# Optimization experiments

Measured on AMD Instinct MI355X. Metric: run time of the kernel, lower is better.

The kernel has to match this reference:

```python
import jax, jax.numpy as jnp
import numpy as np

BETA = 0.25


def setup_inputs() -> dict:
    key = jax.random.key(0)
    k1, k2 = jax.random.split(key)
    x = jax.random.normal(k1, (32, 64, 64, 64), dtype=jnp.float32)   # [B, C, H, W]
    emb = jax.random.normal(k2, (1024, 64), dtype=jnp.float32)       # [K, C] codebook
    return {"x": x, "emb": emb}


def reference(x, emb):
    b, c, h, w = x.shape
    # (b h w) c
    z = jnp.transpose(x, (0, 2, 3, 1)).reshape(-1, c)
    # squared euclidean distances (argmin identical to torch.cdist argmin)
    # ||z||^2 - 2 z e^T + ||e||^2, never taking sqrt since only argmin is used
    d = (jnp.sum(z * z, axis=1, keepdims=True)
         - 2.0 * jnp.einsum('nc,kc->nk', z, emb)
         + jnp.sum(emb * emb, axis=1)[None, :])        # [N, K]
    idx = jnp.argmin(d, axis=1)                        # [N] int
    e = emb[idx]                                       # gather [N, C]
    e = jnp.transpose(e.reshape(b, h, w, c), (0, 3, 1, 2))  # [B, C, H, W]
    codebook_loss = jnp.mean((jax.lax.stop_gradient(x) - e) ** 2)
    commitment_loss = BETA * jnp.mean((x - jax.lax.stop_gradient(e)) ** 2)
    loss = codebook_loss + commitment_loss
    o = x + jax.lax.stop_gradient(e - x)               # straight-through
    indices = idx.reshape(b, h, w)
    return (o, loss, indices)
```

## Files before the change

kernel.cpp:

```cpp
#include <hip/hip_runtime.h>

#define BATCH   32
#define CCH     64
#define HW      4096
#define NPIX    (BATCH * HW)
#define KCODES  1024
#define NELEM   (NPIX * CCH)
#define MB      256
#define CK      128
#define MARGIN_Q 3u

typedef _Float16 f16;
typedef __attribute__((ext_vector_type(8))) _Float16 f16x8;
typedef __attribute__((ext_vector_type(4))) float    f32x4;

static __device__ __forceinline__ f32x4 mfma16(f16x8 a, f16x8 b, f32x4 c) {
    return __builtin_amdgcn_mfma_f32_16x16x32_f16(a, b, c, 0, 0, 0);
}

static __device__ __forceinline__ void dma16(void* lds, const void* g) {
    __builtin_amdgcn_global_load_lds(
        (const __attribute__((address_space(1))) unsigned int*)g,
        (__attribute__((address_space(3))) unsigned int*)lds, 16, 0, 0);
}

static __device__ __forceinline__ unsigned med3u(unsigned a, unsigned b, unsigned c) {
    unsigned d;
    asm("v_med3_u32 %0, %1, %2, %3" : "=v"(d) : "v"(a), "v"(b), "v"(c));
    return d;
}

#define WS_EEB_F   64
#define WS_CBH_B   8192
#define WS_CBL_B   139264
#define WS_WL_U    67584

__global__ __launch_bounds__(256) void vq_prep(
    const float* __restrict__ emb, float* __restrict__ wsf,
    unsigned* __restrict__ wsu, f16* __restrict__ cbH, f16* __restrict__ cbL,
    float* __restrict__ eeb_g)
{
    const int t   = threadIdx.x;
    const int gid = blockIdx.x * 256 + t;
    const int row = gid >> 3, gi = gid & 7;
    if (gid == 0) { wsf[0] = 0.f; wsu[1] = 0u; }
    const float* src = emb + (size_t)row * CCH + gi * 8;
    float4 v0 = *(const float4*)(src);
    float4 v1 = *(const float4*)(src + 4);
    float vv[8] = {v0.x, v0.y, v0.z, v0.w, v1.x, v1.y, v1.z, v1.w};
    f16x8 h, l;
    float s = 0.f;
#pragma unroll
    for (int j = 0; j < 8; ++j) {
        f16 hh = (f16)vv[j];
        h[j] = hh;
        l[j] = (f16)(vv[j] - (float)hh);
        s = fmaf(vv[j], vv[j], s);
    }
    const int off = row * 64 + 8 * (gi ^ (row & 7));
    *(f16x8*)(cbH + off) = h;
    *(f16x8*)(cbL + off) = l;
    s += __shfl_xor(s, 1, 64);
    s += __shfl_xor(s, 2, 64);
    s += __shfl_xor(s, 4, 64);
    if (gi == 0) eeb_g[row] = fmaf(s, 2048.0f, 1048576.0f);
}

__global__ __launch_bounds__(512, 4) void vq_main(
    const float* __restrict__ x,
    const float* __restrict__ emb,
    const f16* __restrict__ cbH, const f16* __restrict__ cbL,
    const float* __restrict__ eeb_g,
    float* __restrict__ o, float* __restrict__ idx_out,
    float* __restrict__ acc, unsigned* __restrict__ wl_count,
    unsigned* __restrict__ wl, unsigned cap)
{
    __shared__ __align__(16) char smem[65536];
    __shared__ float eebl[2][CK];
    __shared__ unsigned bu1[MB], bu2[MB];
    __shared__ float wred[8];

    const int t    = threadIdx.x;
    const int lane = t & 63;
    const int w    = t >> 6;
    const int col  = lane & 15;
    const int quad = lane >> 4;
    const int c7   = col & 7;
    const int sw0  = 8 * (quad ^ c7);
    const int sw1  = sw0 ^ 32;
    const int n0   = blockIdx.x * MB;
    const int b    = n0 >> 12;
    const int p0   = n0 & 4095;
    const float* xb = x + (size_t)b * (CCH * HW) + p0;

    auto stage = [&](int chunk, int bufi) {
        const int k0 = chunk * CK;
        char* lb = smem + bufi * 32768;
        const char* gH = (const char*)cbH + (size_t)k0 * 128 + w * 2048 + lane * 16;
        const char* gL = (const char*)cbL + (size_t)k0 * 128 + w * 2048 + lane * 16;
        char* lH = lb + w * 2048;
        char* lL = lb + 16384 + w * 2048;
        dma16(lH,        gH);
        dma16(lH + 1024, gH + 1024);
        dma16(lL,        gL);
        dma16(lL + 1024, gL + 1024);
        if (t < CK) eebl[bufi][t] = eeb_g[k0 + t];
    };

    stage(0, 0);

    f16x8 aH[2][2], aL[2][2];
#pragma unroll
    for (int rt = 0; rt < 2; ++rt) {
        const int pp = w * 32 + rt * 16 + col;
#pragma unroll
        for (int kc = 0; kc < 2; ++kc) {
            f16x8 h, l;
#pragma unroll
            for (int j = 0; j < 8; ++j) {
                const int c = kc * 32 + quad * 8 + j;
                float zs = -2.0f * xb[(size_t)c * HW + pp];
                f16 hh = (f16)zs;
                h[j] = hh;
                l[j] = (f16)(zs - (float)hh);
            }
            aH[rt][kc] = h;
            aL[rt][kc] = l;
        }
    }

    unsigned best[8], best2[8];
#pragma unroll
    for (int s = 0; s < 8; ++s) { best[s] = 0xFFFFFFFFu; best2[s] = 0xFFFFFFFFu; }

    const f32x4 zero4 = {0.f, 0.f, 0.f, 0.f};

    for (int chunk = 0; chunk < KCODES / CK; ++chunk) {
        const int cur = chunk & 1;
        __syncthreads();
        if (chunk + 1 < KCODES / CK) stage(chunk + 1, cur ^ 1);

        const f16* bufH = (const f16*)(smem + cur * 32768);
        const f16* bufL = bufH + 8192;
        const int k0 = chunk * CK;

#pragma unroll
        for (int tile = 0; tile < CK / 16; ++tile) {
            const f16* bh = bufH + (tile * 16 + col) * 64;
            const f16* bl = bufL + (tile * 16 + col) * 64;
            f16x8 bH0 = *(const f16x8*)(bh + sw0);
            f16x8 bH1 = *(const f16x8*)(bh + sw1);
            f16x8 bL0 = *(const f16x8*)(bl + sw0);
            f16x8 bL1 = *(const f16x8*)(bl + sw1);
            const float eebc = eebl[cur][tile * 16 + col];
            const unsigned kb = (unsigned)(k0 + tile * 16 + col);
#pragma unroll
            for (int rt = 0; rt < 2; ++rt) {
                f32x4 u = mfma16(aH[rt][0], bH0, zero4);
                f32x4 v = mfma16(aH[rt][1], bH1, zero4);
                u = mfma16(aL[rt][0], bH0, u);
                v = mfma16(aL[rt][1], bH1, v);
                u = mfma16(aH[rt][0], bL0, u);
                v = mfma16(aH[rt][1], bL1, v);
#pragma unroll
                for (int r = 0; r < 4; ++r) {
                    float uf = fmaf(u[r] + v[r], 2048.0f, eebc);
                    unsigned pk = (((unsigned)uf) << 10) | kb;
                    const int s = rt * 4 + r;
                    const unsigned b0 = best[s];
                    best2[s] = med3u(b0, best2[s], pk);
                    best[s]  = min(b0, pk);
                }
            }
        }
    }

#pragma unroll
    for (int d = 1; d < 16; d <<= 1) {
#pragma unroll
        for (int s = 0; s < 8; ++s) {
            unsigned ob  = __shfl_xor(best[s],  d, 64);
            unsigned ob2 = __shfl_xor(best2[s], d, 64);
            best2[s] = min(min(best2[s], ob2), max(best[s], ob));
            best[s]  = min(best[s], ob);
        }
    }
    if (col == 0) {
#pragma unroll
        for (int rt = 0; rt < 2; ++rt)
#pragma unroll
            for (int r = 0; r < 4; ++r) {
                const int pl = w * 32 + rt * 16 + quad * 4 + r;
                bu1[pl] = best[rt * 4 + r];
                bu2[pl] = best2[rt * 4 + r];
            }
    }
    __syncthreads();

    const int pix  = t & 255;
    const int half = t >> 8;
    const unsigned bu = bu1[pix];
    const unsigned bidx = bu & 1023u;
    if (half == 0) {
        idx_out[n0 + pix] = (float)bidx;
        const unsigned qg = (bu2[pix] >> 10) - (bu >> 10);
        if (qg < MARGIN_Q) {
            unsigned pos = atomicAdd(wl_count, 1u);
            if (pos < cap) wl[pos] = (unsigned)(n0 + pix);
        }
    }
    float ss = 0.f;
    {
        const float4* er4 = (const float4*)(emb + (size_t)bidx * CCH) + half * 8;
        const float* xbt = xb + pix;
        float* ob = o + (size_t)b * (CCH * HW) + p0 + pix;
#pragma unroll
        for (int i = 0; i < 8; ++i) {
            float4 ev = er4[i];
            float evv[4] = {ev.x, ev.y, ev.z, ev.w};
#pragma unroll
            for (int q = 0; q < 4; ++q) {
                const int c = half * 32 + i * 4 + q;
                float xv = xbt[(size_t)c * HW];
                float e  = evv[q];
                ob[(size_t)c * HW] = xv + (e - xv);
                float d = xv - e;
                ss = fmaf(d, d, ss);
            }
        }
    }
    for (int off = 32; off; off >>= 1) ss += __shfl_down(ss, off, 64);
    if (lane == 0) wred[w] = ss;
    __syncthreads();
    if (t == 0) {
        float s2 = 0.f;
#pragma unroll
        for (int q = 0; q < 8; ++q) s2 += wred[q];
        atomicAdd(acc, s2);
    }
}

__global__ __launch_bounds__(256) void vq_refine(
    const float* __restrict__ x, const float* __restrict__ emb,
    float* __restrict__ o, float* __restrict__ idx_out,
    float* __restrict__ acc, const unsigned* __restrict__ wl_count,
    const unsigned* __restrict__ wl, unsigned cap)
{
    __shared__ float zsh[CCH];
    __shared__ double rbd[4];
    __shared__ int rbi[4];
    __shared__ int s_pk;
    unsigned cnt = *wl_count; if (cnt > cap) cnt = cap;
    const int t = threadIdx.x;

    for (unsigned i = blockIdx.x; i < cnt; i += gridDim.x) {
        const int n = (int)wl[i];
        const int b = n >> 12, p = n & 4095;
        if (t < CCH) zsh[t] = x[(size_t)b * (CCH * HW) + (size_t)t * HW + p];
        __syncthreads();

        double bd = 1e300; int bi = KCODES;
        for (int j = 0; j < 4; ++j) {
            const int k = t + j * 256;
            const float* er = emb + (size_t)k * CCH;
            double d = 0.0;
#pragma unroll
            for (int c = 0; c < CCH; ++c) {
                double tt = (double)zsh[c] - (double)er[c];
                d = fma(tt, tt, d);
            }
            if (d < bd) { bd = d; bi = k; }
        }
        for (int dlt = 1; dlt < 64; dlt <<= 1) {
            double od = __shfl_xor(bd, dlt, 64);
            int    oi = __shfl_xor(bi, dlt, 64);
            if (od < bd || (od == bd && oi < bi)) { bd = od; bi = oi; }
        }
        const int wv = t >> 6;
        if ((t & 63) == 0) { rbd[wv] = bd; rbi[wv] = bi; }
        __syncthreads();
        if (t == 0) {
            double fb = rbd[0]; int fi = rbi[0];
            for (int q = 1; q < 4; ++q)
                if (rbd[q] < fb || (rbd[q] == fb && rbi[q] < fi)) { fb = rbd[q]; fi = rbi[q]; }
            const int old = (int)idx_out[n];
            if (fi != old) { idx_out[n] = (float)fi; s_pk = (old << 16) | fi; }
            else s_pk = -1;
        }
        __syncthreads();
        const int pk = s_pk;
        if (pk >= 0 && t < CCH) {
            const int old = pk >> 16, fi = pk & 0xFFFF;
            const float xv = zsh[t];
            const float eo = emb[(size_t)old * CCH + t];
            const float en = emb[(size_t)fi  * CCH + t];
            o[(size_t)b * (CCH * HW) + (size_t)t * HW + p] = xv + (en - xv);
            const float dn = xv - en, dd = xv - eo;
            float delta = dn * dn - dd * dd;
            for (int off = 32; off; off >>= 1) delta += __shfl_down(delta, off, 64);
            if (t == 0) atomicAdd(acc, delta);
        }
        __syncthreads();
    }
}

__global__ void vq_fin(const float* __restrict__ acc, float* __restrict__ loss) {
    *loss = 1.25f * (*acc) * (1.0f / (float)NELEM);
}

extern "C" void kernel_launch(void* const* d_in, const int* in_sizes, int n_in,
                              void* d_out, int out_size, void* d_ws, size_t ws_size,
                              hipStream_t stream) {
    const float* x   = (const float*)d_in[0];
    const float* emb = (const float*)d_in[1];
    float*    out = (float*)d_out;
    float*    wsf = (float*)d_ws;
    unsigned* wsu = (unsigned*)d_ws;
    char*     wsb = (char*)d_ws;

    float* o_out    = out;
    float* loss_out = out + NELEM;
    float* idx_out  = out + NELEM + 1;
    float* eeb_g    = wsf + WS_EEB_F;
    f16*   cbH      = (f16*)(wsb + WS_CBH_B);
    f16*   cbL      = (f16*)(wsb + WS_CBL_B);
    unsigned* wl    = wsu + WS_WL_U;
    unsigned cap = 0;
    if (ws_size / 4 > WS_WL_U) {
        size_t c = ws_size / 4 - WS_WL_U;
        cap = (unsigned)(c > NPIX ? NPIX : c);
    }

    vq_prep<<<32, 256, 0, stream>>>(emb, wsf, wsu, cbH, cbL, eeb_g);
    vq_main<<<NPIX / MB, 512, 0, stream>>>(x, emb, cbH, cbL, eeb_g, o_out,
                                           idx_out, wsf, wsu + 1, wl, cap);
    vq_refine<<<512, 256, 0, stream>>>(x, emb, o_out, idx_out, wsf,
                                       wsu + 1, wl, cap);
    vq_fin<<<1, 1, 0, stream>>>(wsf, loss_out);
}
```

Before: 153.7 us.

## Fuse ambiguous-pixel fp64 refinement into main kernel, drop refine launch

Pixels whose fp16 distance margin is ambiguous are now re-resolved with exact fp64 distances inside the main kernel, before gather and output, instead of going through a global worklist and a separate refine kernel. This removes one kernel launch, the global atomic worklist, and the patch-up rewrites of output and loss. In exchange, each block serially refines its ambiguous pixels with block-wide syncs, so blocks with many ambiguous pixels stall, and the extra shared memory could lower occupancy.

Result: slower. 245.3 us (+59.6%).

```diff
diff --git a/kernel.cpp b/kernel.cpp
--- a/kernel.cpp
+++ b/kernel.cpp
@@ -33,17 +33,16 @@
 #define WS_EEB_F   64
 #define WS_CBH_B   8192
 #define WS_CBL_B   139264
-#define WS_WL_U    67584
 
 __global__ __launch_bounds__(256) void vq_prep(
     const float* __restrict__ emb, float* __restrict__ wsf,
-    unsigned* __restrict__ wsu, f16* __restrict__ cbH, f16* __restrict__ cbL,
+    f16* __restrict__ cbH, f16* __restrict__ cbL,
     float* __restrict__ eeb_g)
 {
     const int t   = threadIdx.x;
     const int gid = blockIdx.x * 256 + t;
     const int row = gid >> 3, gi = gid & 7;
-    if (gid == 0) { wsf[0] = 0.f; wsu[1] = 0u; }
+    if (gid == 0) { wsf[0] = 0.f; }
     const float* src = emb + (size_t)row * CCH + gi * 8;
     float4 v0 = *(const float4*)(src);
     float4 v1 = *(const float4*)(src + 4);
@@ -72,13 +71,17 @@
     const f16* __restrict__ cbH, const f16* __restrict__ cbL,
     const float* __restrict__ eeb_g,
     float* __restrict__ o, float* __restrict__ idx_out,
-    float* __restrict__ acc, unsigned* __restrict__ wl_count,
-    unsigned* __restrict__ wl, unsigned cap)
+    float* __restrict__ acc)
 {
     __shared__ __align__(16) char smem[65536];
     __shared__ float eebl[2][CK];
     __shared__ unsigned bu1[MB], bu2[MB];
     __shared__ float wred[8];
+    __shared__ unsigned short amb[MB];
+    __shared__ int amb_n;
+    __shared__ float zsh[CCH];
+    __shared__ double rbd[8];
+    __shared__ int rbi[8];
 
     const int t    = threadIdx.x;
     const int lane = t & 63;
@@ -185,6 +188,7 @@
             best[s]  = min(best[s], ob);
         }
     }
+    if (t == 0) amb_n = 0;
     if (col == 0) {
 #pragma unroll
         for (int rt = 0; rt < 2; ++rt)
@@ -197,17 +201,54 @@
     }
     __syncthreads();
 
+    if (t < MB) {
+        const unsigned qg = (bu2[t] >> 10) - (bu1[t] >> 10);
+        if (qg < MARGIN_Q) {
+            int p = atomicAdd(&amb_n, 1);
+            amb[p] = (unsigned short)t;
+        }
+    }
+    __syncthreads();
+    const int na = amb_n;
+    for (int i = 0; i < na; ++i) {
+        const int pix = amb[i];
+        if (t < CCH) zsh[t] = xb[(size_t)t * HW + pix];
+        __syncthreads();
+        double bd = 1e300; int bi = KCODES;
+#pragma unroll
+        for (int j = 0; j < 2; ++j) {
+            const int k = t + j * 512;
+            const float* er = emb + (size_t)k * CCH;
+            double d = 0.0;
+#pragma unroll
+            for (int c = 0; c < CCH; ++c) {
+                double tt = (double)zsh[c] - (double)er[c];
+                d = fma(tt, tt, d);
+            }
+            if (d < bd || (d == bd && k < bi)) { bd = d; bi = k; }
+        }
+#pragma unroll
+        for (int dlt = 1; dlt < 64; dlt <<= 1) {
+            double od = __shfl_xor(bd, dlt, 64);
+            int    oi = __shfl_xor(bi, dlt, 64);
+            if (od < bd || (od == bd && oi < bi)) { bd = od; bi = oi; }
+        }
+        if (lane == 0) { rbd[w] = bd; rbi[w] = bi; }
+        __syncthreads();
+        if (t == 0) {
+            double fb = rbd[0]; int fi = rbi[0];
+            for (int q = 1; q < 8; ++q)
+                if (rbd[q] < fb || (rbd[q] == fb && rbi[q] < fi)) { fb = rbd[q]; fi = rbi[q]; }
+            bu1[pix] = (unsigned)fi;
+        }
+        __syncthreads();
+    }
+
     const int pix  = t & 255;
     const int half = t >> 8;
-    const unsigned bu = bu1[pix];
-    const unsigned bidx = bu & 1023u;
+    const unsigned bidx = bu1[pix] & 1023u;
     if (half == 0) {
         idx_out[n0 + pix] = (float)bidx;
-        const unsigned qg = (bu2[pix] >> 10) - (bu >> 10);
-        if (qg < MARGIN_Q) {
-            unsigned pos = atomicAdd(wl_count, 1u);
-            if (pos < cap) wl[pos] = (unsigned)(n0 + pix);
-        }
     }
     float ss = 0.f;
     {
@@ -240,70 +281,6 @@
     }
 }
 
-__global__ __launch_bounds__(256) void vq_refine(
-    const float* __restrict__ x, const float* __restrict__ emb,
-    float* __restrict__ o, float* __restrict__ idx_out,
-    float* __restrict__ acc, const unsigned* __restrict__ wl_count,
-    const unsigned* __restrict__ wl, unsigned cap)
-{
-    __shared__ float zsh[CCH];
-    __shared__ double rbd[4];
-    __shared__ int rbi[4];
-    __shared__ int s_pk;
-    unsigned cnt = *wl_count; if (cnt > cap) cnt = cap;
-    const int t = threadIdx.x;
-
-    for (unsigned i = blockIdx.x; i < cnt; i += gridDim.x) {
-        const int n = (int)wl[i];
-        const int b = n >> 12, p = n & 4095;
-        if (t < CCH) zsh[t] = x[(size_t)b * (CCH * HW) + (size_t)t * HW + p];
-        __syncthreads();
-
-        double bd = 1e300; int bi = KCODES;
-        for (int j = 0; j < 4; ++j) {
-            const int k = t + j * 256;
-            const float* er = emb + (size_t)k * CCH;
-            double d = 0.0;
-#pragma unroll
-            for (int c = 0; c < CCH; ++c) {
-                double tt = (double)zsh[c] - (double)er[c];
-                d = fma(tt, tt, d);
-            }
-            if (d < bd) { bd = d; bi = k; }
-        }
-        for (int dlt = 1; dlt < 64; dlt <<= 1) {
-            double od = __shfl_xor(bd, dlt, 64);
-            int    oi = __shfl_xor(bi, dlt, 64);
-            if (od < bd || (od == bd && oi < bi)) { bd = od; bi = oi; }
-        }
-        const int wv = t >> 6;
-        if ((t & 63) == 0) { rbd[wv] = bd; rbi[wv] = bi; }
-        __syncthreads();
-        if (t == 0) {
-            double fb = rbd[0]; int fi = rbi[0];
-            for (int q = 1; q < 4; ++q)
-                if (rbd[q] < fb || (rbd[q] == fb && rbi[q] < fi)) { fb = rbd[q]; fi = rbi[q]; }
-            const int old = (int)idx_out[n];
-            if (fi != old) { idx_out[n] = (float)fi; s_pk = (old << 16) | fi; }
-            else s_pk = -1;
-        }
-        __syncthreads();
-        const int pk = s_pk;
-        if (pk >= 0 && t < CCH) {
-            const int old = pk >> 16, fi = pk & 0xFFFF;
-            const float xv = zsh[t];
-            const float eo = emb[(size_t)old * CCH + t];
-            const float en = emb[(size_t)fi  * CCH + t];
-            o[(size_t)b * (CCH * HW) + (size_t)t * HW + p] = xv + (en - xv);
-            const float dn = xv - en, dd = xv - eo;
-            float delta = dn * dn - dd * dd;
-            for (int off = 32; off; off >>= 1) delta += __shfl_down(delta, off, 64);
-            if (t == 0) atomicAdd(acc, delta);
-        }
-        __syncthreads();
-    }
-}
-
 __global__ void vq_fin(const float* __restrict__ acc, float* __restrict__ loss) {
     *loss = 1.25f * (*acc) * (1.0f / (float)NELEM);
 }
@@ -315,7 +292,6 @@
     const float* emb = (const float*)d_in[1];
     float*    out = (float*)d_out;
     float*    wsf = (float*)d_ws;
-    unsigned* wsu = (unsigned*)d_ws;
     char*     wsb = (char*)d_ws;
 
     float* o_out    = out;
@@ -324,17 +300,9 @@
     float* eeb_g    = wsf + WS_EEB_F;
     f16*   cbH      = (f16*)(wsb + WS_CBH_B);
     f16*   cbL      = (f16*)(wsb + WS_CBL_B);
-    unsigned* wl    = wsu + WS_WL_U;
-    unsigned cap = 0;
-    if (ws_size / 4 > WS_WL_U) {
-        size_t c = ws_size / 4 - WS_WL_U;
-        cap = (unsigned)(c > NPIX ? NPIX : c);
-    }
-
-    vq_prep<<<32, 256, 0, stream>>>(emb, wsf, wsu, cbH, cbL, eeb_g);
+
+    vq_prep<<<32, 256, 0, stream>>>(emb, wsf, cbH, cbL, eeb_g);
     vq_main<<<NPIX / MB, 512, 0, stream>>>(x, emb, cbH, cbL, eeb_g, o_out,
-                                           idx_out, wsf, wsu + 1, wl, cap);
-    vq_refine<<<512, 256, 0, stream>>>(x, emb, o_out, idx_out, wsf,
-                                       wsu + 1, wl, cap);
+                                           idx_out, wsf);
     vq_fin<<<1, 1, 0, stream>>>(wsf, loss_out);
 }
```
